# Performance work log

Hardware: AMD Instinct MI355X
Metric: run time of the kernel (lower is better)

Reference implementation:

```python
import jax, jax.numpy as jnp
import numpy as np

DIM = 32
DEPTH = 2  # closed-form Lyndon-basis log-signature implemented for depth 2


def setup_inputs() -> dict:
    key = jax.random.key(0)
    B, L, D = 512, 2048, DIM
    x = jax.random.normal(key, (B, L, D), dtype=jnp.float32)
    return {"x": x}


def _logsig_depth2(x):
    # x: (B, L, D) batch of paths.
    dx = x[:, 1:, :] - x[:, :-1, :]                     # (B, L-1, D) increments
    prefix = jnp.cumsum(dx, axis=1)                      # inclusive prefix sums
    level1 = prefix[:, -1, :]                            # (B, D) total displacement
    prefix_excl = prefix - dx                            # prefix up to t-1 (exclusive)
    # level-2 signature S_ij = sum_t prefix_excl[t, i] * dx[t, j]  -> (B, D, D)
    S2 = jnp.einsum("bli,blj->bij", prefix_excl, dx)
    # log-signature level 2 = antisymmetric part (Levy areas), Lyndon words i<j
    A = 0.5 * (S2 - jnp.swapaxes(S2, 1, 2))             # (B, D, D)
    iu, ju = jnp.triu_indices(x.shape[-1], k=1)          # row-major upper triangle
    areas = A[:, iu, ju]                                 # (B, D*(D-1)/2)
    return jnp.concatenate([level1, areas], axis=-1)     # (B, D + D*(D-1)/2)


def reference(x):
    # Faithful batched equivalent of iisignature.logsig(path, prepare(dim, 2))
    # for every path in the batch (Lyndon basis, depth 2).
    return _logsig_depth2(x)
```

## Files before the change

kernel.cpp:

```cpp
#include <hip/hip_runtime.h>
#include <stdint.h>


constexpr int kB   = 512;
constexpr int kL   = 2048;
constexpr int kD   = 32;
constexpr int kOut = 528;
constexpr int kPan = 32;
constexpr int kTw  = 512;
constexpr int kNP  = kTw / kPan;
constexpr int kCh  = 264;
constexpr int kPB  = 4 * kCh;

typedef __attribute__((ext_vector_type(8))) short bfrag;
typedef __attribute__((ext_vector_type(4))) float f4acc;
union FragU { uint32_t u[4]; bfrag f; };

#if defined(__has_builtin)
#if __has_builtin(__builtin_amdgcn_global_load_lds)
#define LOGSIG_ASYNC_LDS 1
#endif
#endif

__device__ __forceinline__ void async_ld16(const uint32_t* g, uint32_t* l, int lane) {
#ifdef LOGSIG_ASYNC_LDS
    auto* gp = reinterpret_cast<const __attribute__((address_space(1))) uint32_t*>(
        reinterpret_cast<uintptr_t>(g));
    auto* lp = reinterpret_cast<__attribute__((address_space(3))) uint32_t*>(
        reinterpret_cast<uintptr_t>(l));
    __builtin_amdgcn_global_load_lds(gp, lp, 16, 0, 0);
#else
    *(float4*)(l + lane * 4) = *(const float4*)g;
#endif
}

__global__ __launch_bounds__(256, 2)
void logsig_mfma(const float* __restrict__ x, float* __restrict__ out) {
    __shared__ __align__(16) uint32_t sStage[4][2][kPB];
    __shared__ float sx0[kD], sL1[kD];

    const int b     = blockIdx.x;
    const int tid   = threadIdx.x;
    const int wave  = tid >> 6;
    const int lane  = tid & 63;
    const int m     = lane & 15;
    const int q     = lane >> 4;

    const float* __restrict__ xb = x + (size_t)b * (kL * kD);
    const int t0w = wave * kTw;

    auto stage_panel = [&](int p, int buf) {
        uint32_t* dst = &sStage[wave][buf][0];
        const int rbase = t0w + p * kPan;
        #pragma unroll
        for (int c = 0; c < 4; ++c) {
            int r = rbase + c * 8 + (lane >> 3);
            r = r < kL - 1 ? r : kL - 1;
            const uint32_t* g = (const uint32_t*)xb + (size_t)r * kD + (lane & 7) * 4;
            async_ld16(g, dst + c * kCh, lane);
        }
    };

    f4acc acc[4];
    #pragma unroll
    for (int t = 0; t < 4; ++t)
        #pragma unroll
        for (int e = 0; e < 4; ++e) acc[t][e] = 0.0f;

    auto make_frags = [&](const uint32_t* e, FragU& AH, FragU& AL,
                          FragU& BH, FragU& BL) {
        uint32_t l[9];
        #pragma unroll
        for (int j = 0; j < 9; ++j) {
            const uint32_t fh = e[j] & 0xffff0000u;
            const float r = __builtin_bit_cast(float, e[j])
                          - __builtin_bit_cast(float, fh);
            l[j] = __builtin_bit_cast(uint32_t, r);
        }
        #pragma unroll
        for (int d = 0; d < 4; ++d) {
            AH.u[d] = __builtin_amdgcn_perm(e[2*d+1], e[2*d],   0x07060302u);
            AL.u[d] = __builtin_amdgcn_perm(l[2*d+1], l[2*d],   0x07060302u);
            BH.u[d] = __builtin_amdgcn_perm(e[2*d+2], e[2*d+1], 0x07060302u);
            BL.u[d] = __builtin_amdgcn_perm(l[2*d+2], l[2*d+1], 0x07060302u);
        }
    };

    stage_panel(0, 0);

    #pragma unroll
    for (int p = 0; p < kNP; ++p) {
        const int cu = p & 1, nb = cu ^ 1;

        uint32_t h0 = 0, h1 = 0;
        if (p == kNP - 1) {
            int hr = t0w + kTw;
            hr = hr < kL - 1 ? hr : kL - 1;
            const uint32_t* g = (const uint32_t*)xb + (size_t)hr * kD;
            h0 = g[m];
            h1 = g[m + 16];
        }

        if (p + 1 < kNP) {
            stage_panel(p + 1, nb);
            asm volatile("s_waitcnt vmcnt(3)" ::: "memory");
        } else {
            asm volatile("s_waitcnt vmcnt(0)" ::: "memory");
        }

        const uint32_t* sb = &sStage[wave][cu][0];
        uint32_t e0[9], e1[9];
        #pragma unroll
        for (int j = 0; j < 8; ++j) {
            const int a = q * kCh + j * 32 + m;
            e0[j] = sb[a];
            e1[j] = sb[a + 16];
        }
        if (p == kNP - 1 && q == 3) {
            e0[8] = h0;
            e1[8] = h1;
        } else {
            const uint32_t* hb = (q < 3) ? sb + (q + 1) * kCh
                                         : &sStage[wave][nb][0];
            e0[8] = hb[m];
            e1[8] = hb[m + 16];
        }

        FragU A0H, A0L, B0H, B0L, A1H, A1L, B1H, B1L;
        make_frags(e0, A0H, A0L, B0H, B0L);
        make_frags(e1, A1H, A1L, B1H, B1L);

        acc[0] = __builtin_amdgcn_mfma_f32_16x16x32_bf16(A0H.f, B0H.f, acc[0], 0, 0, 0);
        acc[0] = __builtin_amdgcn_mfma_f32_16x16x32_bf16(A0H.f, B0L.f, acc[0], 0, 0, 0);
        acc[0] = __builtin_amdgcn_mfma_f32_16x16x32_bf16(A0L.f, B0H.f, acc[0], 0, 0, 0);
        acc[1] = __builtin_amdgcn_mfma_f32_16x16x32_bf16(A0H.f, B1H.f, acc[1], 0, 0, 0);
        acc[1] = __builtin_amdgcn_mfma_f32_16x16x32_bf16(A0H.f, B1L.f, acc[1], 0, 0, 0);
        acc[1] = __builtin_amdgcn_mfma_f32_16x16x32_bf16(A0L.f, B1H.f, acc[1], 0, 0, 0);
        acc[2] = __builtin_amdgcn_mfma_f32_16x16x32_bf16(A1H.f, B0H.f, acc[2], 0, 0, 0);
        acc[2] = __builtin_amdgcn_mfma_f32_16x16x32_bf16(A1H.f, B0L.f, acc[2], 0, 0, 0);
        acc[2] = __builtin_amdgcn_mfma_f32_16x16x32_bf16(A1L.f, B0H.f, acc[2], 0, 0, 0);
        acc[3] = __builtin_amdgcn_mfma_f32_16x16x32_bf16(A1H.f, B1H.f, acc[3], 0, 0, 0);
        acc[3] = __builtin_amdgcn_mfma_f32_16x16x32_bf16(A1H.f, B1L.f, acc[3], 0, 0, 0);
        acc[3] = __builtin_amdgcn_mfma_f32_16x16x32_bf16(A1L.f, B1H.f, acc[3], 0, 0, 0);
    }

    float* sWw = (float*)&sStage[wave][0][0];
    #pragma unroll
    for (int t = 0; t < 4; ++t) {
        const int tr = t >> 1, tc = t & 1;
        #pragma unroll
        for (int e = 0; e < 4; ++e) {
            const int row = 16 * tr + q * 4 + e;
            const int col = 16 * tc + m;
            sWw[row * kD + col] = acc[t][e];
        }
    }
    if (tid < kD) {
        const float x0v = xb[tid];
        const float xev = xb[(size_t)(kL - 1) * kD + tid];
        sx0[tid] = x0v;
        sL1[tid] = xev - x0v;
    }
    __syncthreads();

    float* sW0 = (float*)&sStage[0][0][0];
    for (int c = tid; c < kD * kD; c += 256)
        sW0[c] += ((float*)&sStage[1][0][0])[c]
                + ((float*)&sStage[2][0][0])[c]
                + ((float*)&sStage[3][0][0])[c];
    __syncthreads();

    float* ob = out + (size_t)b * kOut;
    for (int o = tid; o < kOut; o += 256) {
        if (o < 32) {
            ob[o] = sL1[o];
        } else {
            int p = o - 32, i = 0;
            while (p >= 31 - i) { p -= 31 - i; ++i; }
            const int j = i + 1 + p;
            float v = 0.5f * (sW0[i * kD + j] - sW0[j * kD + i])
                    + 0.5f * (sx0[j] * sL1[i] - sx0[i] * sL1[j]);
            ob[o] = v;
        }
    }
}

extern "C" void kernel_launch(void* const* d_in, const int* in_sizes, int n_in,
                              void* d_out, int out_size, void* d_ws, size_t ws_size,
                              hipStream_t stream) {
    const float* x = (const float*)d_in[0];
    float* out = (float*)d_out;
    logsig_mfma<<<dim3(kB), dim3(256), 0, stream>>>(x, out);
}
```

Before: 191.1 us.

## Replace async global-to-LDS staging with 3-deep register prefetch pipeline

Drops the global_load_lds async copies and explicit vmcnt waits. Panels are now loaded into registers three panels ahead, then written to the LDS double buffer. The halo row for each quarter is also fetched directly from global memory every panel instead of being read from the neighbouring LDS region. The aim is deeper latency hiding with compiler-managed waits, at the cost of more VGPRs (three sets of u32x4[4]) and extra global halo loads per panel, which could hurt occupancy under launch_bounds(256,2). The last-row clamp was also dropped from the main loads, which appears safe because rows never exceed kL-1.

```diff
diff --git a/kernel.cpp b/kernel.cpp
--- a/kernel.cpp
+++ b/kernel.cpp
@@ -14,51 +14,47 @@
 
 typedef __attribute__((ext_vector_type(8))) short bfrag;
 typedef __attribute__((ext_vector_type(4))) float f4acc;
+typedef __attribute__((ext_vector_type(4))) uint32_t u32x4;
 union FragU { uint32_t u[4]; bfrag f; };
-
-#if defined(__has_builtin)
-#if __has_builtin(__builtin_amdgcn_global_load_lds)
-#define LOGSIG_ASYNC_LDS 1
-#endif
-#endif
-
-__device__ __forceinline__ void async_ld16(const uint32_t* g, uint32_t* l, int lane) {
-#ifdef LOGSIG_ASYNC_LDS
-    auto* gp = reinterpret_cast<const __attribute__((address_space(1))) uint32_t*>(
-        reinterpret_cast<uintptr_t>(g));
-    auto* lp = reinterpret_cast<__attribute__((address_space(3))) uint32_t*>(
-        reinterpret_cast<uintptr_t>(l));
-    __builtin_amdgcn_global_load_lds(gp, lp, 16, 0, 0);
-#else
-    *(float4*)(l + lane * 4) = *(const float4*)g;
-#endif
-}
 
 __global__ __launch_bounds__(256, 2)
 void logsig_mfma(const float* __restrict__ x, float* __restrict__ out) {
     __shared__ __align__(16) uint32_t sStage[4][2][kPB];
     __shared__ float sx0[kD], sL1[kD];
 
-    const int b     = blockIdx.x;
-    const int tid   = threadIdx.x;
-    const int wave  = tid >> 6;
-    const int lane  = tid & 63;
-    const int m     = lane & 15;
-    const int q     = lane >> 4;
+    const int b    = blockIdx.x;
+    const int tid  = threadIdx.x;
+    const int wave = tid >> 6;
+    const int lane = tid & 63;
+    const int m    = lane & 15;
+    const int q    = lane >> 4;
 
     const float* __restrict__ xb = x + (size_t)b * (kL * kD);
-    const int t0w = wave * kTw;
+    const int t0w  = wave * kTw;
+    const int grow = lane >> 3;
+    const int gcol = (lane & 7) * 4;
 
-    auto stage_panel = [&](int p, int buf) {
-        uint32_t* dst = &sStage[wave][buf][0];
+    auto issue_g = [&](int p, u32x4 (&g)[4]) {
         const int rbase = t0w + p * kPan;
         #pragma unroll
         for (int c = 0; c < 4; ++c) {
-            int r = rbase + c * 8 + (lane >> 3);
-            r = r < kL - 1 ? r : kL - 1;
-            const uint32_t* g = (const uint32_t*)xb + (size_t)r * kD + (lane & 7) * 4;
-            async_ld16(g, dst + c * kCh, lane);
+            const uint32_t* gp = (const uint32_t*)xb
+                               + (size_t)(rbase + c * 8 + grow) * kD + gcol;
+            g[c] = *(const u32x4*)gp;
         }
+    };
+    auto write_g = [&](const u32x4 (&g)[4], int buf) {
+        uint32_t* dst = &sStage[wave][buf][0];
+        #pragma unroll
+        for (int c = 0; c < 4; ++c)
+            *(u32x4*)(dst + c * kCh + lane * 4) = g[c];
+    };
+    auto issue_h = [&](int p, uint32_t& h0, uint32_t& h1) {
+        int hr = t0w + p * kPan + q * 8 + 8;
+        hr = hr < kL - 1 ? hr : kL - 1;
+        const uint32_t* gp = (const uint32_t*)xb + (size_t)hr * kD;
+        h0 = gp[m];
+        h1 = gp[m + 16];
     };
 
     f4acc acc[4];
@@ -86,27 +82,19 @@
         }
     };
 
-    stage_panel(0, 0);
+    u32x4 g[4], g2[4], g3[4];
+    issue_g(0, g);
+    write_g(g, 0);
+    issue_g(1, g);
+    issue_g(2, g2);
 
     #pragma unroll
     for (int p = 0; p < kNP; ++p) {
         const int cu = p & 1, nb = cu ^ 1;
 
-        uint32_t h0 = 0, h1 = 0;
-        if (p == kNP - 1) {
-            int hr = t0w + kTw;
-            hr = hr < kL - 1 ? hr : kL - 1;
-            const uint32_t* g = (const uint32_t*)xb + (size_t)hr * kD;
-            h0 = g[m];
-            h1 = g[m + 16];
-        }
-
-        if (p + 1 < kNP) {
-            stage_panel(p + 1, nb);
-            asm volatile("s_waitcnt vmcnt(3)" ::: "memory");
-        } else {
-            asm volatile("s_waitcnt vmcnt(0)" ::: "memory");
-        }
+        uint32_t h0, h1;
+        issue_h(p, h0, h1);
+        if (p + 3 < kNP) issue_g(p + 3, g3);
 
         const uint32_t* sb = &sStage[wave][cu][0];
         uint32_t e0[9], e1[9];
@@ -116,15 +104,19 @@
             e0[j] = sb[a];
             e1[j] = sb[a + 16];
         }
-        if (p == kNP - 1 && q == 3) {
-            e0[8] = h0;
-            e1[8] = h1;
-        } else {
-            const uint32_t* hb = (q < 3) ? sb + (q + 1) * kCh
-                                         : &sStage[wave][nb][0];
-            e0[8] = hb[m];
-            e1[8] = hb[m + 16];
+
+        if (p + 1 < kNP) write_g(g, nb);
+        if (p + 2 < kNP) {
+            #pragma unroll
+            for (int c = 0; c < 4; ++c) g[c] = g2[c];
         }
+        if (p + 3 < kNP) {
+            #pragma unroll
+            for (int c = 0; c < 4; ++c) g2[c] = g3[c];
+        }
+
+        e0[8] = h0;
+        e1[8] = h1;
 
         FragU A0H, A0L, B0H, B0L, A1H, A1L, B1H, B1L;
         make_frags(e0, A0H, A0L, B0H, B0L);
```

New measurement: 191.2 us. No clear change (+0.0%).
